# Performance work log

Measured on AMD Instinct MI355X. Metric: run time of the kernel, lower is better.

The kernel has to match this reference:

```python
import jax, jax.numpy as jnp
from jax import lax
import numpy as np

B, S, D, T = 64, 1024, 1024, 32  # batch, seq_len, encoder_dim, num_tags


def setup_inputs():
    key = jax.random.key(0)
    ks = jax.random.split(key, 5)
    logits = jax.random.normal(ks[0], (B, S, D), dtype=jnp.float32)
    mask = jnp.ones((B, S), dtype=bool)
    W = jax.random.normal(ks[1], (T, D), dtype=jnp.float32) / np.sqrt(D).astype(np.float32)
    b = jnp.zeros((T,), dtype=jnp.float32)
    transitions = jax.random.normal(ks[2], (T, T), dtype=jnp.float32) * 0.1
    start_transitions = jax.random.normal(ks[3], (T,), dtype=jnp.float32) * 0.1
    end_transitions = jax.random.normal(ks[4], (T,), dtype=jnp.float32) * 0.1
    return dict(logits=logits, mask=mask, W=W, b=b, transitions=transitions,
                start_transitions=start_transitions, end_transitions=end_transitions)


def _viterbi(emissions, mask, transitions, start_t, end_t):
    # emissions: [B,S,T] tag scores; mask: [B,S] bool. Returns best tag path [B,S].
    Tn = emissions.shape[-1]
    score0 = start_t[None, :] + emissions[:, 0]  # [B,T]

    def step(score, xs):
        emit_t, m_t = xs  # [B,T], [B]
        cand = score[:, :, None] + transitions[None]  # [B, prev_tag, cur_tag]
        best_score = jnp.max(cand, axis=1) + emit_t   # [B,T]
        best_prev = jnp.argmax(cand, axis=1)          # [B,T]
        m = m_t[:, None]
        new_score = jnp.where(m, best_score, score)
        bp = jnp.where(m, best_prev, jnp.arange(Tn)[None, :])  # masked step: self-loop
        return new_score, bp

    emits = jnp.swapaxes(emissions[:, 1:], 0, 1)  # [S-1,B,T]
    masks = jnp.swapaxes(mask[:, 1:], 0, 1)       # [S-1,B]
    final, bps = lax.scan(step, score0, (emits, masks))
    final = final + end_t[None, :]
    last_tag = jnp.argmax(final, axis=-1)  # [B]

    def back(tag, bp):
        prev = jnp.take_along_axis(bp, tag[:, None], axis=1)[:, 0]
        return prev, tag  # emit tag at this position, carry previous tag

    first_tag, tail = lax.scan(back, last_tag, bps, reverse=True)
    return jnp.concatenate([first_tag[:, None], jnp.swapaxes(tail, 0, 1)], axis=1)  # [B,S]


def reference(logits, mask, W, b, transitions, start_transitions, end_transitions):
    # linear projection to tag space
    linear_logits = jnp.einsum('bsd,td->bst', logits, W) + b  # [B,S,T]
    # CRF Viterbi decode
    tags = _viterbi(linear_logits, mask, transitions, start_transitions, end_transitions)
    # _broadcast_tags: one-hot scatter of the decoded path (only at unmasked positions)
    crf_logits = jax.nn.one_hot(tags, linear_logits.shape[-1], dtype=linear_logits.dtype) \
        * mask[:, :, None].astype(linear_logits.dtype)
    return (linear_logits, crf_logits)
```

## Files before the change

### kernel.cpp

```cpp
#include <hip/hip_runtime.h>

#define BB 64
#define SS 1024
#define DD 1024
#define TT 32

__global__ __launch_bounds__(256)
__attribute__((amdgpu_waves_per_eu(1, 4)))
void gemm_slice(const float* __restrict__ L, const float* __restrict__ Wm,
                float* __restrict__ part)
{
    __shared__ __align__(16) float wt[256 * TT];

    const int tid = threadIdx.x;
    const int rb = blockIdx.x & 255;
    const int ks = blockIdx.x >> 8;
    const int kbase = ks << 8;

    {
        const int t  = tid >> 3;
        const int dg = tid & 7;
        const float* wrow = Wm + (size_t)t * DD + kbase;
#pragma unroll
        for (int kk = 0; kk < 8; ++kk) {
            int dl = dg * 4 + kk * 32;
            float4 v = *reinterpret_cast<const float4*>(wrow + dl);
            wt[(dl + 0) * TT + t] = v.x;
            wt[(dl + 1) * TT + t] = v.y;
            wt[(dl + 2) * TT + t] = v.z;
            wt[(dl + 3) * TT + t] = v.w;
        }
    }
    __syncthreads();

    const int wave = tid >> 6, lane = tid & 63;
    const int o = lane & 7;
    const int g = lane >> 3;
    const int rowbase = rb * 256 + wave * 64 + g;
    const float* Lr = L + (size_t)rowbase * DD + kbase;

    float4 acc[8];
#pragma unroll
    for (int m = 0; m < 8; ++m) acc[m] = make_float4(0.f, 0.f, 0.f, 0.f);

    float4 a0[8], a1[8];
#pragma unroll
    for (int m = 0; m < 8; ++m) {
        const float* rp = Lr + (size_t)m * 8 * DD;
        a0[m] = *reinterpret_cast<const float4*>(rp + 0);
        a1[m] = *reinterpret_cast<const float4*>(rp + 4);
    }

    auto do_phase = [&](float4 (&buf)[8], int lp) {
        float4 w[4];
#pragma unroll
        for (int kk = 0; kk < 4; ++kk)
            w[kk] = *reinterpret_cast<const float4*>(&wt[(lp * 4 + kk) * TT + o * 4]);
#pragma unroll
        for (int m = 0; m < 8; ++m) {
            float4 a = buf[m];
            acc[m].x = fmaf(a.x, w[0].x, acc[m].x);
            acc[m].y = fmaf(a.x, w[0].y, acc[m].y);
            acc[m].z = fmaf(a.x, w[0].z, acc[m].z);
            acc[m].w = fmaf(a.x, w[0].w, acc[m].w);
            acc[m].x = fmaf(a.y, w[1].x, acc[m].x);
            acc[m].y = fmaf(a.y, w[1].y, acc[m].y);
            acc[m].z = fmaf(a.y, w[1].z, acc[m].z);
            acc[m].w = fmaf(a.y, w[1].w, acc[m].w);
            acc[m].x = fmaf(a.z, w[2].x, acc[m].x);
            acc[m].y = fmaf(a.z, w[2].y, acc[m].y);
            acc[m].z = fmaf(a.z, w[2].z, acc[m].z);
            acc[m].w = fmaf(a.z, w[2].w, acc[m].w);
            acc[m].x = fmaf(a.w, w[3].x, acc[m].x);
            acc[m].y = fmaf(a.w, w[3].y, acc[m].y);
            acc[m].z = fmaf(a.w, w[3].z, acc[m].z);
            acc[m].w = fmaf(a.w, w[3].w, acc[m].w);
        }
        const int pf = lp + 2;
        if (pf < 64) {
#pragma unroll
            for (int m = 0; m < 8; ++m)
                buf[m] = *reinterpret_cast<const float4*>(
                    Lr + (size_t)m * 8 * DD + pf * 4);
        }
    };

#pragma unroll 2
    for (int pp = 0; pp < 64; pp += 2) {
        do_phase(a0, pp);
        do_phase(a1, pp + 1);
    }

    float* pb = part + (size_t)ks * (65536 * TT);
#pragma unroll
    for (int m = 0; m < 8; ++m)
        *reinterpret_cast<float4*>(
            pb + (size_t)(rowbase + m * 8) * TT + o * 4) = acc[m];
}

__global__ __launch_bounds__(256) void reduce4(
    const float* __restrict__ part, const float* __restrict__ bias,
    float* __restrict__ out)
{
    const int i = blockIdx.x * 256 + threadIdx.x;
    const float4* p4 = reinterpret_cast<const float4*>(part);
    float4 s0 = p4[i];
    float4 s1 = p4[i + 524288];
    float4 s2 = p4[i + 2 * 524288];
    float4 s3 = p4[i + 3 * 524288];
    float4 b4 = reinterpret_cast<const float4*>(bias)[i & 7];
    float4 r;
    r.x = (s0.x + s1.x) + (s2.x + s3.x) + b4.x;
    r.y = (s0.y + s1.y) + (s2.y + s3.y) + b4.y;
    r.z = (s0.z + s1.z) + (s2.z + s3.z) + b4.z;
    r.w = (s0.w + s1.w) + (s2.w + s3.w) + b4.w;
    reinterpret_cast<float4*>(out)[i] = r;
}

__global__ __launch_bounds__(256) void gemm_full(
    const float* __restrict__ L, const float* __restrict__ Wm,
    const float* __restrict__ bias, float* __restrict__ out)
{
    __shared__ __align__(16) float wt[256 * TT];

    const int tid  = threadIdx.x;
    const int lane = tid & 63, wave = tid >> 6;
    const int o = lane & 7;
    const int g = lane >> 3;
    const int rowbase = blockIdx.x * 256 + wave * 64 + g;
    const float* Lr = L + (size_t)rowbase * DD;

    const int wt_t  = tid >> 3;
    const int wt_dg = tid & 7;
    const float* wrow = Wm + (size_t)wt_t * DD;

    float4 b4 = *reinterpret_cast<const float4*>(bias + o * 4);
    float4 acc[8];
#pragma unroll
    for (int m = 0; m < 8; ++m) acc[m] = b4;

    float4 a0[8], a1[8];
#pragma unroll
    for (int m = 0; m < 8; ++m) {
        const float* rp = Lr + (size_t)m * 8 * DD;
        a0[m] = *reinterpret_cast<const float4*>(rp + 0);
        a1[m] = *reinterpret_cast<const float4*>(rp + 4);
    }

    auto do_phase = [&](float4 (&buf)[8], int gp, int lp) {
        float4 w[4];
#pragma unroll
        for (int kk = 0; kk < 4; ++kk)
            w[kk] = *reinterpret_cast<const float4*>(&wt[(lp * 4 + kk) * TT + o * 4]);
#pragma unroll
        for (int m = 0; m < 8; ++m) {
            float4 a = buf[m];
            acc[m].x = fmaf(a.x, w[0].x, acc[m].x);
            acc[m].y = fmaf(a.x, w[0].y, acc[m].y);
            acc[m].z = fmaf(a.x, w[0].z, acc[m].z);
            acc[m].w = fmaf(a.x, w[0].w, acc[m].w);
            acc[m].x = fmaf(a.y, w[1].x, acc[m].x);
            acc[m].y = fmaf(a.y, w[1].y, acc[m].y);
            acc[m].z = fmaf(a.y, w[1].z, acc[m].z);
            acc[m].w = fmaf(a.y, w[1].w, acc[m].w);
            acc[m].x = fmaf(a.z, w[2].x, acc[m].x);
            acc[m].y = fmaf(a.z, w[2].y, acc[m].y);
            acc[m].z = fmaf(a.z, w[2].z, acc[m].z);
            acc[m].w = fmaf(a.z, w[2].w, acc[m].w);
            acc[m].x = fmaf(a.w, w[3].x, acc[m].x);
            acc[m].y = fmaf(a.w, w[3].y, acc[m].y);
            acc[m].z = fmaf(a.w, w[3].z, acc[m].z);
            acc[m].w = fmaf(a.w, w[3].w, acc[m].w);
        }
        const int pf = gp + 2;
        if (pf < 256) {
#pragma unroll
            for (int m = 0; m < 8; ++m)
                buf[m] = *reinterpret_cast<const float4*>(
                    Lr + (size_t)m * 8 * DD + pf * 4);
        }
    };

    for (int tile = 0; tile < 4; ++tile) {
        if (tile) __syncthreads();
#pragma unroll
        for (int kk = 0; kk < 8; ++kk) {
            int dl = wt_dg * 4 + kk * 32;
            float4 v = *reinterpret_cast<const float4*>(wrow + tile * 256 + dl);
            wt[(dl + 0) * TT + wt_t] = v.x;
            wt[(dl + 1) * TT + wt_t] = v.y;
            wt[(dl + 2) * TT + wt_t] = v.z;
            wt[(dl + 3) * TT + wt_t] = v.w;
        }
        __syncthreads();

        const int p4base = tile * 64;
#pragma unroll 2
        for (int pp = 0; pp < 64; pp += 2) {
            do_phase(a0, p4base + pp, pp);
            do_phase(a1, p4base + pp + 1, pp + 1);
        }
    }

#pragma unroll
    for (int m = 0; m < 8; ++m)
        *reinterpret_cast<float4*>(out + (size_t)(rowbase + m * 8) * TT + o * 4) = acc[m];
}

__global__ __launch_bounds__(512) void viterbi_defer2(
    const float* __restrict__ emis, const float* __restrict__ trans,
    const float* __restrict__ startt, const float* __restrict__ endt,
    float* __restrict__ crf, float* __restrict__ ws_scores)
{
    __shared__ unsigned char bp[(SS - 1) * TT];
    __shared__ unsigned char exits[16 * TT];
    __shared__ unsigned char tags[SS];
    __shared__ int entryc[16];
    __shared__ int lastTag;
    __shared__ __align__(16) float srow[TT];

    const int tid = threadIdx.x;
    const int b = blockIdx.x;
    const float* eb = emis + (size_t)b * SS * TT;
    float* wsb = ws_scores + (size_t)b * (SS - 1) * TT;

    if (tid < 64) {
        const int j = tid & 31;
        const int h = tid >> 5;
        float tr[16];
#pragma unroll
        for (int i = 0; i < 16; ++i) tr[i] = trans[(h * 16 + i) * TT + j];

        float ns = startt[j] + eb[j];

        float ec[8], en[8];
#pragma unroll
        for (int t = 0; t < 8; ++t) ec[t] = eb[(1 + t) * TT + j];

        float* wp = wsb + j;

        for (int s0 = 1; s0 < SS; s0 += 8) {
#pragma unroll
            for (int t = 0; t < 8; ++t) {
                int sp = s0 + 8 + t; sp = sp > SS - 1 ? SS - 1 : sp;
                en[t] = eb[sp * TT + j];
            }
#pragma unroll
            for (int t = 0; t < 8; ++t) {
                const int s = s0 + t;
                if (s < SS) {
                    *wp = ns; wp += TT;
                    srow[j] = ns;
                    float sc[16];
#pragma unroll
                    for (int q = 0; q < 4; ++q)
                        *reinterpret_cast<float4*>(&sc[q * 4]) =
                            *reinterpret_cast<const float4*>(&srow[h * 16 + q * 4]);
                    float c[16];
#pragma unroll
                    for (int i = 0; i < 16; ++i) c[i] = sc[i] + tr[i];
                    float m0 = fmaxf(fmaxf(c[0],  c[1]),  c[2]);
                    float m1 = fmaxf(fmaxf(c[3],  c[4]),  c[5]);
                    float m2 = fmaxf(fmaxf(c[6],  c[7]),  c[8]);
                    float m3 = fmaxf(fmaxf(c[9],  c[10]), c[11]);
                    float m4 = fmaxf(fmaxf(c[12], c[13]), c[14]);
                    float n0 = fmaxf(fmaxf(m0, m1), m2);
                    float n1 = fmaxf(fmaxf(m3, m4), c[15]);
                    float halfmax = fmaxf(n0, n1);
#if __has_builtin(__builtin_amdgcn_permlane32_swap)
                    unsigned hu = __builtin_bit_cast(unsigned, halfmax);
                    auto pr = __builtin_amdgcn_permlane32_swap(hu, hu, false, false);
                    float full = fmaxf(__builtin_bit_cast(float, (unsigned)pr[0]),
                                       __builtin_bit_cast(float, (unsigned)pr[1]));
#else
                    float full = fmaxf(halfmax, __shfl_xor(halfmax, 32, 64));
#endif
                    ns = full + ec[t];
                }
            }
#pragma unroll
            for (int t = 0; t < 8; ++t) ec[t] = en[t];
        }

        float fin = ns + endt[j];
        int ji = j;
#pragma unroll
        for (int m = 1; m < 32; m <<= 1) {
            float ov = __shfl_xor(fin, m, 64);
            int   oi = __shfl_xor(ji, m, 64);
            bool take = (fin > ov) || (fin == ov && ji < oi);
            fin = take ? fin : ov;
            ji  = take ? ji  : oi;
        }
        if (tid == 0) lastTag = ji;
    }
    __syncthreads();

    {
        const int j = tid & 31;
        const int g = tid >> 5;
        float tr[32];
#pragma unroll
        for (int i = 0; i < 32; ++i) tr[i] = trans[i * TT + j];

        for (int r = 0; r < 64; ++r) {
            int s = 1 + g + (r << 4);
            if (s < SS) {
                const float* sr = wsb + (size_t)(s - 1) * TT;
                float sc[32];
#pragma unroll
                for (int q = 0; q < 8; ++q)
                    *reinterpret_cast<float4*>(&sc[q * 4]) =
                        *reinterpret_cast<const float4*>(sr + q * 4);
                float bv = sc[0] + tr[0]; int bi = 0;
#pragma unroll
                for (int i = 1; i < 32; ++i) {
                    float cd = sc[i] + tr[i];
                    bool gt = cd > bv;
                    bv = gt ? cd : bv;
                    bi = gt ? i : bi;
                }
                bp[(s - 1) * TT + j] = (unsigned char)bi;
            }
        }
    }
    __syncthreads();

    {
        const int c = tid >> 5, jj = tid & 31;
        int t = jj;
#pragma unroll 1
        for (int k = 0; k < 64; ++k) {
            int s = c * 64 + 63 - k;
            if (s >= 1) t = bp[(s - 1) * TT + t];
        }
        exits[c * TT + jj] = (unsigned char)t;
    }
    __syncthreads();

    if (tid == 0) {
        int t = lastTag;
        for (int c = 15; c >= 0; --c) { entryc[c] = t; t = exits[c * TT + t]; }
    }
    __syncthreads();

    if (tid < 16) {
        const int c = tid;
        int t = entryc[c];
#pragma unroll 1
        for (int k = 0; k < 64; ++k) {
            int s = c * 64 + 63 - k;
            tags[s] = (unsigned char)t;
            if (s >= 1) t = bp[(s - 1) * TT + t];
        }
    }
    __syncthreads();

    float* cb = crf + (size_t)b * SS * TT;
#pragma unroll
    for (int i = 0; i < 16; ++i) {
        int fi = tid + 512 * i;
        int s = fi >> 3, q = fi & 7;
        int tag = tags[s];
        float4 v;
        v.x = (q * 4 + 0 == tag) ? 1.0f : 0.0f;
        v.y = (q * 4 + 1 == tag) ? 1.0f : 0.0f;
        v.z = (q * 4 + 2 == tag) ? 1.0f : 0.0f;
        v.w = (q * 4 + 3 == tag) ? 1.0f : 0.0f;
        *reinterpret_cast<float4*>(cb + (size_t)fi * 4) = v;
    }
}

__global__ __launch_bounds__(512) void viterbi_inline(
    const float* __restrict__ emis, const float* __restrict__ trans,
    const float* __restrict__ startt, const float* __restrict__ endt,
    float* __restrict__ crf)
{
    __shared__ unsigned char bp[SS * TT];
    __shared__ unsigned char exits[16 * TT];
    __shared__ unsigned char tags[SS];
    __shared__ int entryc[16];
    __shared__ int lastTag;

    const int tid = threadIdx.x;
    const int b = blockIdx.x;
    const float* eb = emis + (size_t)b * SS * TT;

    if (tid < 64) {
        const int lane = tid;
        const int j = lane & 31;
        const int h = lane >> 5;
        const bool hlo = (h == 0);
        const int hbase = h << 4;

        float tr[16];
#pragma unroll
        for (int ii = 0; ii < 16; ++ii) tr[ii] = trans[(hbase + ii) * TT + j];

        float ns = startt[j] + eb[j];

        float ecur[4];
#pragma unroll
        for (int t = 0; t < 4; ++t) ecur[t] = eb[(1 + t) * TT + j];

        for (int s0 = 1; s0 < SS; s0 += 4) {
            float enx[4];
#pragma unroll
            for (int t = 0; t < 4; ++t) {
                int sp = s0 + 4 + t; if (sp > SS - 1) sp = SS - 1;
                enx[t] = eb[sp * TT + j];
            }
#pragma unroll
            for (int t = 0; t < 4; ++t) {
                const int s = s0 + t;
                if (s < SS) {
                    float c[16];
#pragma unroll
                    for (int ii = 0; ii < 16; ++ii)
                        c[ii] = __shfl(ns, hbase + ii, 64) + tr[ii];
                    float v8[8]; int i8[8];
#pragma unroll
                    for (int p = 0; p < 8; ++p) {
                        bool gg = c[2*p] >= c[2*p+1];
                        v8[p] = gg ? c[2*p] : c[2*p+1];
                        i8[p] = gg ? (2*p) : (2*p+1);
                    }
                    float v4[4]; int i4[4];
#pragma unroll
                    for (int p = 0; p < 4; ++p) {
                        bool gg = v8[2*p] >= v8[2*p+1];
                        v4[p] = gg ? v8[2*p] : v8[2*p+1];
                        i4[p] = gg ? i8[2*p] : i8[2*p+1];
                    }
                    float v2[2]; int i2[2];
#pragma unroll
                    for (int p = 0; p < 2; ++p) {
                        bool gg = v4[2*p] >= v4[2*p+1];
                        v2[p] = gg ? v4[2*p] : v4[2*p+1];
                        i2[p] = gg ? i4[2*p] : i4[2*p+1];
                    }
                    bool gb = v2[0] >= v2[1];
                    float vb = gb ? v2[0] : v2[1];
                    int ib = (gb ? i2[0] : i2[1]) + hbase;

                    float ov = __shfl_xor(vb, 32, 64);
                    int   oi = __shfl_xor(ib, 32, 64);
                    float vLow  = hlo ? vb : ov;
                    int   iLow  = hlo ? ib : oi;
                    float vHigh = hlo ? ov : vb;
                    int   iHigh = hlo ? oi : ib;
                    bool gg = vLow >= vHigh;
                    float bestv = gg ? vLow : vHigh;
                    int   besti = gg ? iLow : iHigh;

                    ns = bestv + ecur[t];
                    bp[s * TT + j] = (unsigned char)besti;
                }
            }
#pragma unroll
            for (int t = 0; t < 4; ++t) ecur[t] = enx[t];
        }

        float fin = ns + endt[j];
        int ji = j;
#pragma unroll
        for (int m = 1; m < 32; m <<= 1) {
            float ov = __shfl_xor(fin, m, 64);
            int   oi = __shfl_xor(ji, m, 64);
            bool take = (fin > ov) || (fin == ov && ji < oi);
            fin = take ? fin : ov;
            ji  = take ? ji  : oi;
        }
        if (lane == 0) lastTag = ji;
    }
    __syncthreads();

    {
        const int c = tid >> 5, jj = tid & 31;
        int t = jj;
#pragma unroll 1
        for (int k = 0; k < 64; ++k) {
            int s = c * 64 + 63 - k;
            if (s >= 1) t = bp[s * TT + t];
        }
        exits[c * TT + jj] = (unsigned char)t;
    }
    __syncthreads();

    if (tid == 0) {
        int t = lastTag;
        for (int c = 15; c >= 0; --c) { entryc[c] = t; t = exits[c * TT + t]; }
    }
    __syncthreads();

    if (tid < 16) {
        const int c = tid;
        int t = entryc[c];
#pragma unroll 1
        for (int k = 0; k < 64; ++k) {
            int s = c * 64 + 63 - k;
            tags[s] = (unsigned char)t;
            if (s >= 1) t = bp[s * TT + t];
        }
    }
    __syncthreads();

    float* cb = crf + (size_t)b * SS * TT;
#pragma unroll
    for (int i = 0; i < 16; ++i) {
        int fi = tid + 512 * i;
        int s = fi >> 3, q = fi & 7;
        int tag = tags[s];
        float4 v;
        v.x = (q * 4 + 0 == tag) ? 1.0f : 0.0f;
        v.y = (q * 4 + 1 == tag) ? 1.0f : 0.0f;
        v.z = (q * 4 + 2 == tag) ? 1.0f : 0.0f;
        v.w = (q * 4 + 3 == tag) ? 1.0f : 0.0f;
        *reinterpret_cast<float4*>(cb + (size_t)fi * 4) = v;
    }
}

extern "C" void kernel_launch(void* const* d_in, const int* in_sizes, int n_in,
                              void* d_out, int out_size, void* d_ws, size_t ws_size,
                              hipStream_t stream)
{
    const float* logits = (const float*)d_in[0];
    const float* W      = (const float*)d_in[2];
    const float* bias   = (const float*)d_in[3];
    const float* trans  = (const float*)d_in[4];
    const float* startt = (const float*)d_in[5];
    const float* endt   = (const float*)d_in[6];

    float* out = (float*)d_out;
    float* crf = out + (size_t)BB * SS * TT;

    const size_t need_split  = (size_t)4 * 65536 * TT * sizeof(float);
    const size_t need_scores = (size_t)BB * (SS - 1) * TT * sizeof(float);

    if (ws_size >= need_split) {
        gemm_slice<<<1024, 256, 0, stream>>>(logits, W, (float*)d_ws);
        reduce4<<<2048, 256, 0, stream>>>((const float*)d_ws, bias, out);
        viterbi_defer2<<<BB, 512, 0, stream>>>(out, trans, startt, endt, crf,
                                               (float*)d_ws);
    } else if (ws_size >= need_scores) {
        gemm_full<<<256, 256, 0, stream>>>(logits, W, bias, out);
        viterbi_defer2<<<BB, 512, 0, stream>>>(out, trans, startt, endt, crf,
                                               (float*)d_ws);
    } else {
        gemm_full<<<256, 256, 0, stream>>>(logits, W, bias, out);
        viterbi_inline<<<BB, 512, 0, stream>>>(out, trans, startt, endt, crf);
    }
}
```

Measured before the change: 291.3 us.

## Widen split-K GEMM to 512 threads and use bpermute in Viterbi recurrence

The split-K GEMM slice kernel now runs 512 threads per block, each thread computing 4 consecutive rows instead of 8 strided rows. This roughly halves the per-thread register footprint and doubles the waves available to hide latency. The Viterbi forward loop drops the shared-memory score row and its write/read round trip, and instead gathers the previous scores across lanes with ds_bpermute. That removes an LDS store-load dependency from the serial critical path, but issues 16 bpermute operations per step instead of 4 vector LDS reads.

```diff
diff --git a/kernel.cpp b/kernel.cpp
--- a/kernel.cpp
+++ b/kernel.cpp
@@ -5,10 +5,10 @@
 #define DD 1024
 #define TT 32
 
-__global__ __launch_bounds__(256)
+__global__ __launch_bounds__(512)
 __attribute__((amdgpu_waves_per_eu(1, 4)))
-void gemm_slice(const float* __restrict__ L, const float* __restrict__ Wm,
-                float* __restrict__ part)
+void gemm_slice512(const float* __restrict__ L, const float* __restrict__ Wm,
+                   float* __restrict__ part)
 {
     __shared__ __align__(16) float wt[256 * TT];
 
@@ -18,12 +18,12 @@
     const int kbase = ks << 8;
 
     {
-        const int t  = tid >> 3;
-        const int dg = tid & 7;
+        const int t  = tid >> 4;
+        const int dg = tid & 15;
         const float* wrow = Wm + (size_t)t * DD + kbase;
 #pragma unroll
-        for (int kk = 0; kk < 8; ++kk) {
-            int dl = dg * 4 + kk * 32;
+        for (int c = 0; c < 4; ++c) {
+            int dl = dg * 4 + c * 64;
             float4 v = *reinterpret_cast<const float4*>(wrow + dl);
             wt[(dl + 0) * TT + t] = v.x;
             wt[(dl + 1) * TT + t] = v.y;
@@ -33,15 +33,110 @@
     }
     __syncthreads();
 
-    const int wave = tid >> 6, lane = tid & 63;
+    const int o = tid & 7;
+    const int g = tid >> 3;
+    const int rowbase = rb * 256 + g * 4;
+    const float* Lr = L + (size_t)rowbase * DD + kbase;
+
+    float4 acc[4];
+#pragma unroll
+    for (int m = 0; m < 4; ++m) acc[m] = make_float4(0.f, 0.f, 0.f, 0.f);
+
+    float4 a0[4], a1[4];
+#pragma unroll
+    for (int m = 0; m < 4; ++m) {
+        const float* rp = Lr + (size_t)m * DD;
+        a0[m] = *reinterpret_cast<const float4*>(rp + 0);
+        a1[m] = *reinterpret_cast<const float4*>(rp + 4);
+    }
+
+    auto do_phase = [&](float4 (&buf)[4], int lp) {
+        float4 w[4];
+#pragma unroll
+        for (int kk = 0; kk < 4; ++kk)
+            w[kk] = *reinterpret_cast<const float4*>(&wt[(lp * 4 + kk) * TT + o * 4]);
+#pragma unroll
+        for (int m = 0; m < 4; ++m) {
+            float4 a = buf[m];
+            acc[m].x = fmaf(a.x, w[0].x, acc[m].x);
+            acc[m].y = fmaf(a.x, w[0].y, acc[m].y);
+            acc[m].z = fmaf(a.x, w[0].z, acc[m].z);
+            acc[m].w = fmaf(a.x, w[0].w, acc[m].w);
+            acc[m].x = fmaf(a.y, w[1].x, acc[m].x);
+            acc[m].y = fmaf(a.y, w[1].y, acc[m].y);
+            acc[m].z = fmaf(a.y, w[1].z, acc[m].z);
+            acc[m].w = fmaf(a.y, w[1].w, acc[m].w);
+            acc[m].x = fmaf(a.z, w[2].x, acc[m].x);
+            acc[m].y = fmaf(a.z, w[2].y, acc[m].y);
+            acc[m].z = fmaf(a.z, w[2].z, acc[m].z);
+            acc[m].w = fmaf(a.z, w[2].w, acc[m].w);
+            acc[m].x = fmaf(a.w, w[3].x, acc[m].x);
+            acc[m].y = fmaf(a.w, w[3].y, acc[m].y);
+            acc[m].z = fmaf(a.w, w[3].z, acc[m].z);
+            acc[m].w = fmaf(a.w, w[3].w, acc[m].w);
+        }
+        const int pf = lp + 2;
+        if (pf < 64) {
+#pragma unroll
+            for (int m = 0; m < 4; ++m)
+                buf[m] = *reinterpret_cast<const float4*>(
+                    Lr + (size_t)m * DD + pf * 4);
+        }
+    };
+
+#pragma unroll 2
+    for (int pp = 0; pp < 64; pp += 2) {
+        do_phase(a0, pp);
+        do_phase(a1, pp + 1);
+    }
+
+    float* pb = part + (size_t)ks * (65536 * TT);
+#pragma unroll
+    for (int m = 0; m < 4; ++m)
+        *reinterpret_cast<float4*>(
+            pb + (size_t)(rowbase + m) * TT + o * 4) = acc[m];
+}
+
+__global__ __launch_bounds__(256) void reduce4(
+    const float* __restrict__ part, const float* __restrict__ bias,
+    float* __restrict__ out)
+{
+    const int i = blockIdx.x * 256 + threadIdx.x;
+    const float4* p4 = reinterpret_cast<const float4*>(part);
+    float4 s0 = p4[i];
+    float4 s1 = p4[i + 524288];
+    float4 s2 = p4[i + 2 * 524288];
+    float4 s3 = p4[i + 3 * 524288];
+    float4 b4 = reinterpret_cast<const float4*>(bias)[i & 7];
+    float4 r;
+    r.x = (s0.x + s1.x) + (s2.x + s3.x) + b4.x;
+    r.y = (s0.y + s1.y) + (s2.y + s3.y) + b4.y;
+    r.z = (s0.z + s1.z) + (s2.z + s3.z) + b4.z;
+    r.w = (s0.w + s1.w) + (s2.w + s3.w) + b4.w;
+    reinterpret_cast<float4*>(out)[i] = r;
+}
+
+__global__ __launch_bounds__(256) void gemm_full(
+    const float* __restrict__ L, const float* __restrict__ Wm,
+    const float* __restrict__ bias, float* __restrict__ out)
+{
+    __shared__ __align__(16) float wt[256 * TT];
+
+    const int tid  = threadIdx.x;
+    const int lane = tid & 63, wave = tid >> 6;
     const int o = lane & 7;
     const int g = lane >> 3;
-    const int rowbase = rb * 256 + wave * 64 + g;
-    const float* Lr = L + (size_t)rowbase * DD + kbase;
-
+    const int rowbase = blockIdx.x * 256 + wave * 64 + g;
+    const float* Lr = L + (size_t)rowbase * DD;
+
+    const int wt_t  = tid >> 3;
+    const int wt_dg = tid & 7;
+    const float* wrow = Wm + (size_t)wt_t * DD;
+
+    float4 b4 = *reinterpret_cast<const float4*>(bias + o * 4);
     float4 acc[8];
 #pragma unroll
-    for (int m = 0; m < 8; ++m) acc[m] = make_float4(0.f, 0.f, 0.f, 0.f);
+    for (int m = 0; m < 8; ++m) acc[m] = b4;
 
     float4 a0[8], a1[8];
 #pragma unroll
@@ -51,7 +146,7 @@
         a1[m] = *reinterpret_cast<const float4*>(rp + 4);
     }
 
-    auto do_phase = [&](float4 (&buf)[8], int lp) {
+    auto do_phase = [&](float4 (&buf)[8], int gp, int lp) {
         float4 w[4];
 #pragma unroll
         for (int kk = 0; kk < 4; ++kk)
@@ -76,102 +171,6 @@
             acc[m].z = fmaf(a.w, w[3].z, acc[m].z);
             acc[m].w = fmaf(a.w, w[3].w, acc[m].w);
         }
-        const int pf = lp + 2;
-        if (pf < 64) {
-#pragma unroll
-            for (int m = 0; m < 8; ++m)
-                buf[m] = *reinterpret_cast<const float4*>(
-                    Lr + (size_t)m * 8 * DD + pf * 4);
-        }
-    };
-
-#pragma unroll 2
-    for (int pp = 0; pp < 64; pp += 2) {
-        do_phase(a0, pp);
-        do_phase(a1, pp + 1);
-    }
-
-    float* pb = part + (size_t)ks * (65536 * TT);
-#pragma unroll
-    for (int m = 0; m < 8; ++m)
-        *reinterpret_cast<float4*>(
-            pb + (size_t)(rowbase + m * 8) * TT + o * 4) = acc[m];
-}
-
-__global__ __launch_bounds__(256) void reduce4(
-    const float* __restrict__ part, const float* __restrict__ bias,
-    float* __restrict__ out)
-{
-    const int i = blockIdx.x * 256 + threadIdx.x;
-    const float4* p4 = reinterpret_cast<const float4*>(part);
-    float4 s0 = p4[i];
-    float4 s1 = p4[i + 524288];
-    float4 s2 = p4[i + 2 * 524288];
-    float4 s3 = p4[i + 3 * 524288];
-    float4 b4 = reinterpret_cast<const float4*>(bias)[i & 7];
-    float4 r;
-    r.x = (s0.x + s1.x) + (s2.x + s3.x) + b4.x;
-    r.y = (s0.y + s1.y) + (s2.y + s3.y) + b4.y;
-    r.z = (s0.z + s1.z) + (s2.z + s3.z) + b4.z;
-    r.w = (s0.w + s1.w) + (s2.w + s3.w) + b4.w;
-    reinterpret_cast<float4*>(out)[i] = r;
-}
-
-__global__ __launch_bounds__(256) void gemm_full(
-    const float* __restrict__ L, const float* __restrict__ Wm,
-    const float* __restrict__ bias, float* __restrict__ out)
-{
-    __shared__ __align__(16) float wt[256 * TT];
-
-    const int tid  = threadIdx.x;
-    const int lane = tid & 63, wave = tid >> 6;
-    const int o = lane & 7;
-    const int g = lane >> 3;
-    const int rowbase = blockIdx.x * 256 + wave * 64 + g;
-    const float* Lr = L + (size_t)rowbase * DD;
-
-    const int wt_t  = tid >> 3;
-    const int wt_dg = tid & 7;
-    const float* wrow = Wm + (size_t)wt_t * DD;
-
-    float4 b4 = *reinterpret_cast<const float4*>(bias + o * 4);
-    float4 acc[8];
-#pragma unroll
-    for (int m = 0; m < 8; ++m) acc[m] = b4;
-
-    float4 a0[8], a1[8];
-#pragma unroll
-    for (int m = 0; m < 8; ++m) {
-        const float* rp = Lr + (size_t)m * 8 * DD;
-        a0[m] = *reinterpret_cast<const float4*>(rp + 0);
-        a1[m] = *reinterpret_cast<const float4*>(rp + 4);
-    }
-
-    auto do_phase = [&](float4 (&buf)[8], int gp, int lp) {
-        float4 w[4];
-#pragma unroll
-        for (int kk = 0; kk < 4; ++kk)
-            w[kk] = *reinterpret_cast<const float4*>(&wt[(lp * 4 + kk) * TT + o * 4]);
-#pragma unroll
-        for (int m = 0; m < 8; ++m) {
-            float4 a = buf[m];
-            acc[m].x = fmaf(a.x, w[0].x, acc[m].x);
-            acc[m].y = fmaf(a.x, w[0].y, acc[m].y);
-            acc[m].z = fmaf(a.x, w[0].z, acc[m].z);
-            acc[m].w = fmaf(a.x, w[0].w, acc[m].w);
-            acc[m].x = fmaf(a.y, w[1].x, acc[m].x);
-            acc[m].y = fmaf(a.y, w[1].y, acc[m].y);
-            acc[m].z = fmaf(a.y, w[1].z, acc[m].z);
-            acc[m].w = fmaf(a.y, w[1].w, acc[m].w);
-            acc[m].x = fmaf(a.z, w[2].x, acc[m].x);
-            acc[m].y = fmaf(a.z, w[2].y, acc[m].y);
-            acc[m].z = fmaf(a.z, w[2].z, acc[m].z);
-            acc[m].w = fmaf(a.z, w[2].w, acc[m].w);
-            acc[m].x = fmaf(a.w, w[3].x, acc[m].x);
-            acc[m].y = fmaf(a.w, w[3].y, acc[m].y);
-            acc[m].z = fmaf(a.w, w[3].z, acc[m].z);
-            acc[m].w = fmaf(a.w, w[3].w, acc[m].w);
-        }
         const int pf = gp + 2;
         if (pf < 256) {
 #pragma unroll
@@ -207,7 +206,7 @@
         *reinterpret_cast<float4*>(out + (size_t)(rowbase + m * 8) * TT + o * 4) = acc[m];
 }
 
-__global__ __launch_bounds__(512) void viterbi_defer2(
+__global__ __launch_bounds__(512) void viterbi_defer3(
     const float* __restrict__ emis, const float* __restrict__ trans,
     const float* __restrict__ startt, const float* __restrict__ endt,
     float* __restrict__ crf, float* __restrict__ ws_scores)
@@ -217,7 +216,6 @@
     __shared__ unsigned char tags[SS];
     __shared__ int entryc[16];
     __shared__ int lastTag;
-    __shared__ __align__(16) float srow[TT];
 
     const int tid = threadIdx.x;
     const int b = blockIdx.x;
@@ -227,9 +225,11 @@
     if (tid < 64) {
         const int j = tid & 31;
         const int h = tid >> 5;
+        const int hbase = h << 4;
+        const int baddr = hbase << 2;
         float tr[16];
 #pragma unroll
-        for (int i = 0; i < 16; ++i) tr[i] = trans[(h * 16 + i) * TT + j];
+        for (int i = 0; i < 16; ++i) tr[i] = trans[(hbase + i) * TT + j];
 
         float ns = startt[j] + eb[j];
 
@@ -250,15 +250,13 @@
                 const int s = s0 + t;
                 if (s < SS) {
                     *wp = ns; wp += TT;
-                    srow[j] = ns;
-                    float sc[16];
-#pragma unroll
-                    for (int q = 0; q < 4; ++q)
-                        *reinterpret_cast<float4*>(&sc[q * 4]) =
-                            *reinterpret_cast<const float4*>(&srow[h * 16 + q * 4]);
                     float c[16];
-#pragma unroll
-                    for (int i = 0; i < 16; ++i) c[i] = sc[i] + tr[i];
+                    int nsu = __builtin_bit_cast(int, ns);
+#pragma unroll
+                    for (int n = 0; n < 16; ++n) {
+                        int gv = __builtin_amdgcn_ds_bpermute(baddr + 4 * n, nsu);
+                        c[n] = __builtin_bit_cast(float, gv) + tr[n];
+                    }
                     float m0 = fmaxf(fmaxf(c[0],  c[1]),  c[2]);
                     float m1 = fmaxf(fmaxf(c[3],  c[4]),  c[5]);
                     float m2 = fmaxf(fmaxf(c[6],  c[7]),  c[8]);
@@ -538,13 +536,13 @@
     const size_t need_scores = (size_t)BB * (SS - 1) * TT * sizeof(float);
 
     if (ws_size >= need_split) {
-        gemm_slice<<<1024, 256, 0, stream>>>(logits, W, (float*)d_ws);
+        gemm_slice512<<<1024, 512, 0, stream>>>(logits, W, (float*)d_ws);
         reduce4<<<2048, 256, 0, stream>>>((const float*)d_ws, bias, out);
-        viterbi_defer2<<<BB, 512, 0, stream>>>(out, trans, startt, endt, crf,
+        viterbi_defer3<<<BB, 512, 0, stream>>>(out, trans, startt, endt, crf,
                                                (float*)d_ws);
     } else if (ws_size >= need_scores) {
         gemm_full<<<256, 256, 0, stream>>>(logits, W, bias, out);
-        viterbi_defer2<<<BB, 512, 0, stream>>>(out, trans, startt, endt, crf,
+        viterbi_defer3<<<BB, 512, 0, stream>>>(out, trans, startt, endt, crf,
                                                (float*)d_ws);
     } else {
         gemm_full<<<256, 256, 0, stream>>>(logits, W, bias, out);
```

After: 354.9 us. 1.22x slower.

## Restructure split-K projection GEMM with smaller per-thread tiles and swizzled LDS

Applied to the files above, without the earlier changes.

Rewrites the split-K projection kernel so each thread holds 2 rows instead of 8, with 512-thread blocks and twice as many blocks. The weight tile in shared memory gets an XOR swizzle to avoid bank conflicts, and the input stream now keeps 4 float4 buffers in flight instead of 2 for deeper prefetch. The aim is higher occupancy and better latency hiding on the memory-bound logits stream. The cost is less reuse of each weight value loaded from LDS, so LDS traffic per FMA goes up.

```diff
diff --git a/kernel.cpp b/kernel.cpp
--- a/kernel.cpp
+++ b/kernel.cpp
@@ -5,97 +5,101 @@
 #define DD 1024
 #define TT 32
 
-__global__ __launch_bounds__(256)
+__global__ __launch_bounds__(512)
 __attribute__((amdgpu_waves_per_eu(1, 4)))
-void gemm_slice(const float* __restrict__ L, const float* __restrict__ Wm,
-                float* __restrict__ part)
+void gemm_slice_v3(const float* __restrict__ L, const float* __restrict__ Wm,
+                   float* __restrict__ part)
 {
     __shared__ __align__(16) float wt[256 * TT];
 
     const int tid = threadIdx.x;
-    const int rb = blockIdx.x & 255;
-    const int ks = blockIdx.x >> 8;
+    const int rb = blockIdx.x & 511;
+    const int ks = blockIdx.x >> 9;
     const int kbase = ks << 8;
 
     {
-        const int t  = tid >> 3;
-        const int dg = tid & 7;
+        const int t  = tid >> 4;
+        const int dg = tid & 15;
+        const int q = t >> 2, tb = t & 3;
         const float* wrow = Wm + (size_t)t * DD + kbase;
 #pragma unroll
-        for (int kk = 0; kk < 8; ++kk) {
-            int dl = dg * 4 + kk * 32;
+        for (int c = 0; c < 4; ++c) {
+            int dl = dg * 4 + c * 64;
             float4 v = *reinterpret_cast<const float4*>(wrow + dl);
-            wt[(dl + 0) * TT + t] = v.x;
-            wt[(dl + 1) * TT + t] = v.y;
-            wt[(dl + 2) * TT + t] = v.z;
-            wt[(dl + 3) * TT + t] = v.w;
-        }
-    }
-    __syncthreads();
-
-    const int wave = tid >> 6, lane = tid & 63;
-    const int o = lane & 7;
-    const int g = lane >> 3;
-    const int rowbase = rb * 256 + wave * 64 + g;
-    const float* Lr = L + (size_t)rowbase * DD + kbase;
-
-    float4 acc[8];
-#pragma unroll
-    for (int m = 0; m < 8; ++m) acc[m] = make_float4(0.f, 0.f, 0.f, 0.f);
-
-    float4 a0[8], a1[8];
-#pragma unroll
-    for (int m = 0; m < 8; ++m) {
-        const float* rp = Lr + (size_t)m * 8 * DD;
-        a0[m] = *reinterpret_cast<const float4*>(rp + 0);
-        a1[m] = *reinterpret_cast<const float4*>(rp + 4);
-    }
-
-    auto do_phase = [&](float4 (&buf)[8], int lp) {
-        float4 w[4];
-#pragma unroll
-        for (int kk = 0; kk < 4; ++kk)
-            w[kk] = *reinterpret_cast<const float4*>(&wt[(lp * 4 + kk) * TT + o * 4]);
-#pragma unroll
-        for (int m = 0; m < 8; ++m) {
-            float4 a = buf[m];
-            acc[m].x = fmaf(a.x, w[0].x, acc[m].x);
-            acc[m].y = fmaf(a.x, w[0].y, acc[m].y);
-            acc[m].z = fmaf(a.x, w[0].z, acc[m].z);
-            acc[m].w = fmaf(a.x, w[0].w, acc[m].w);
-            acc[m].x = fmaf(a.y, w[1].x, acc[m].x);
-            acc[m].y = fmaf(a.y, w[1].y, acc[m].y);
-            acc[m].z = fmaf(a.y, w[1].z, acc[m].z);
-            acc[m].w = fmaf(a.y, w[1].w, acc[m].w);
-            acc[m].x = fmaf(a.z, w[2].x, acc[m].x);
-            acc[m].y = fmaf(a.z, w[2].y, acc[m].y);
-            acc[m].z = fmaf(a.z, w[2].z, acc[m].z);
-            acc[m].w = fmaf(a.z, w[2].w, acc[m].w);
-            acc[m].x = fmaf(a.w, w[3].x, acc[m].x);
-            acc[m].y = fmaf(a.w, w[3].y, acc[m].y);
-            acc[m].z = fmaf(a.w, w[3].z, acc[m].z);
-            acc[m].w = fmaf(a.w, w[3].w, acc[m].w);
-        }
-        const int pf = lp + 2;
+            int col = ((q ^ ((dl >> 2) & 7)) << 2) + tb;
+            wt[(dl + 0) * TT + col] = v.x;
+            wt[(dl + 1) * TT + col] = v.y;
+            wt[(dl + 2) * TT + col] = v.z;
+            wt[(dl + 3) * TT + col] = v.w;
+        }
+    }
+    __syncthreads();
+
+    const int o = tid & 7;
+    const int g = tid >> 3;
+    const int rowbase = rb * 128 + g * 2;
+    const float* Lr0 = L + (size_t)rowbase * DD + kbase;
+    const float* Lr1 = Lr0 + DD;
+
+    float4 acc0 = make_float4(0.f, 0.f, 0.f, 0.f);
+    float4 acc1 = make_float4(0.f, 0.f, 0.f, 0.f);
+
+    float4 B0[2], B1[2], B2[2], B3[2];
+    B0[0] = *reinterpret_cast<const float4*>(Lr0 + 0);
+    B0[1] = *reinterpret_cast<const float4*>(Lr1 + 0);
+    B1[0] = *reinterpret_cast<const float4*>(Lr0 + 4);
+    B1[1] = *reinterpret_cast<const float4*>(Lr1 + 4);
+    B2[0] = *reinterpret_cast<const float4*>(Lr0 + 8);
+    B2[1] = *reinterpret_cast<const float4*>(Lr1 + 8);
+    B3[0] = *reinterpret_cast<const float4*>(Lr0 + 12);
+    B3[1] = *reinterpret_cast<const float4*>(Lr1 + 12);
+
+    auto phase = [&](float4 (&B)[2], int lp) {
+        const int key = lp & 7;
+        const float* wb = &wt[(lp * 4) * TT + ((o ^ key) << 2)];
+        float4 w0 = *reinterpret_cast<const float4*>(wb);
+        float4 w1 = *reinterpret_cast<const float4*>(wb + TT);
+        float4 w2 = *reinterpret_cast<const float4*>(wb + 2 * TT);
+        float4 w3 = *reinterpret_cast<const float4*>(wb + 3 * TT);
+#pragma unroll
+        for (int m = 0; m < 2; ++m) {
+            float4 a = B[m];
+            float4& ac = m ? acc1 : acc0;
+            ac.x = fmaf(a.x, w0.x, ac.x);
+            ac.y = fmaf(a.x, w0.y, ac.y);
+            ac.z = fmaf(a.x, w0.z, ac.z);
+            ac.w = fmaf(a.x, w0.w, ac.w);
+            ac.x = fmaf(a.y, w1.x, ac.x);
+            ac.y = fmaf(a.y, w1.y, ac.y);
+            ac.z = fmaf(a.y, w1.z, ac.z);
+            ac.w = fmaf(a.y, w1.w, ac.w);
+            ac.x = fmaf(a.z, w2.x, ac.x);
+            ac.y = fmaf(a.z, w2.y, ac.y);
+            ac.z = fmaf(a.z, w2.z, ac.z);
+            ac.w = fmaf(a.z, w2.w, ac.w);
+            ac.x = fmaf(a.w, w3.x, ac.x);
+            ac.y = fmaf(a.w, w3.y, ac.y);
+            ac.z = fmaf(a.w, w3.z, ac.z);
+            ac.w = fmaf(a.w, w3.w, ac.w);
+        }
+        const int pf = lp + 4;
         if (pf < 64) {
-#pragma unroll
-            for (int m = 0; m < 8; ++m)
-                buf[m] = *reinterpret_cast<const float4*>(
-                    Lr + (size_t)m * 8 * DD + pf * 4);
+            B[0] = *reinterpret_cast<const float4*>(Lr0 + pf * 4);
+            B[1] = *reinterpret_cast<const float4*>(Lr1 + pf * 4);
         }
     };
 
-#pragma unroll 2
-    for (int pp = 0; pp < 64; pp += 2) {
-        do_phase(a0, pp);
-        do_phase(a1, pp + 1);
+#pragma unroll 1
+    for (int pp = 0; pp < 64; pp += 4) {
+        phase(B0, pp + 0);
+        phase(B1, pp + 1);
+        phase(B2, pp + 2);
+        phase(B3, pp + 3);
     }
 
     float* pb = part + (size_t)ks * (65536 * TT);
-#pragma unroll
-    for (int m = 0; m < 8; ++m)
-        *reinterpret_cast<float4*>(
-            pb + (size_t)(rowbase + m * 8) * TT + o * 4) = acc[m];
+    *reinterpret_cast<float4*>(pb + (size_t)rowbase * TT + o * 4) = acc0;
+    *reinterpret_cast<float4*>(pb + (size_t)(rowbase + 1) * TT + o * 4) = acc1;
 }
 
 __global__ __launch_bounds__(256) void reduce4(
@@ -538,7 +542,7 @@
     const size_t need_scores = (size_t)BB * (SS - 1) * TT * sizeof(float);
 
     if (ws_size >= need_split) {
-        gemm_slice<<<1024, 256, 0, stream>>>(logits, W, (float*)d_ws);
+        gemm_slice_v3<<<2048, 512, 0, stream>>>(logits, W, (float*)d_ws);
         reduce4<<<2048, 256, 0, stream>>>((const float*)d_ws, bias, out);
         viterbi_defer2<<<BB, 512, 0, stream>>>(out, trans, startt, endt, crf,
                                                (float*)d_ws);
```

Result: faster. 284.7 us (-2.3%).
